# Optimization experiments

Hardware: AMD Instinct MI355X
Metric: run time of the kernel (lower is better)

The kernel has to match this reference:

```python
import jax, jax.numpy as jnp
import numpy as np
from jax import lax

Z, Y, X = 9, 5, 5          # anchor grid (AnchorInit)
A = Z * Y * X              # 225 anchors
NS = 8                     # nsample in AnchorGrouping
H = 64                     # feature / hidden width


def anchor_template():
    # (Z,Y,X,3) grid of anchor coordinates, last dim ordered (x,y,z) so that
    # anchors[:,:,:2] += g_loc shifts the planar (x,y) location.
    xs = (jnp.arange(X, dtype=jnp.float32) - (X - 1) / 2.0) * 0.2
    ys = (jnp.arange(Y, dtype=jnp.float32) - (Y - 1) / 2.0) * 0.2
    zs = jnp.arange(Z, dtype=jnp.float32) * 0.22 + 0.1
    gz, gy, gx = jnp.meshgrid(zs, ys, xs, indexing='ij')
    return jnp.stack([gx, gy, gz], axis=-1)


def setup_inputs() -> dict:
    key = jax.random.key(0)
    ks = jax.random.split(key, 16)
    B, T, N, F = 16, 64, 128, 2
    M = B * T
    s = 0.1
    f32 = jnp.float32
    return {
        'x': jax.random.normal(ks[0], (M, N, 3 + F), f32),
        'g_loc': jax.random.normal(ks[1], (B, T, 2), f32) * 0.5,
        'h0': jnp.zeros((1, B, H), f32),
        'c0': jnp.zeros((1, B, H), f32),
        # AnchorPointNet: per-point MLP 5->16->32->64 + attention pooling
        'pn_w1': jax.random.normal(ks[2], (3 + F, 16), f32) * s,
        'pn_b1': jnp.zeros((16,), f32),
        'pn_w2': jax.random.normal(ks[3], (16, 32), f32) * s,
        'pn_b2': jnp.zeros((32,), f32),
        'pn_w3': jax.random.normal(ks[4], (32, H), f32) * s,
        'pn_b3': jnp.zeros((H,), f32),
        'attn_w': jax.random.normal(ks[5], (H, 1), f32) * s,
        'attn_b': jnp.zeros((1,), f32),
        # AnchorVoxelNet: Conv3d 64->96 (3,3,3), 96->128 (3,3,3), 128->64 (5,1,1), OIDHW
        'vx_w1': jax.random.normal(ks[6], (96, 64, 3, 3, 3), f32) * s,
        'vx_b1': jnp.zeros((96,), f32),
        'vx_w2': jax.random.normal(ks[7], (128, 96, 3, 3, 3), f32) * s,
        'vx_b2': jnp.zeros((128,), f32),
        'vx_w3': jax.random.normal(ks[8], (64, 128, 5, 1, 1), f32) * s,
        'vx_b3': jnp.zeros((64,), f32),
        # AnchorRNN: 1-layer LSTM, input 64, hidden 64, torch gate order (i,f,g,o)
        'lstm_wi': jax.random.normal(ks[9], (H, 4 * H), f32) * s,
        'lstm_wh': jax.random.normal(ks[10], (H, 4 * H), f32) * s,
        'lstm_b': jnp.zeros((4 * H,), f32),
        'batch_size': 16,
        'length_size': 64,
        'feature_size': 2,
    }


def reference(x, g_loc, h0, c0,
              pn_w1, pn_b1, pn_w2, pn_b2, pn_w3, pn_b3, attn_w, attn_b,
              vx_w1, vx_b1, vx_w2, vx_b2, vx_w3, vx_b3,
              lstm_wi, lstm_wh, lstm_b,
              batch_size, length_size, feature_size):
    M = batch_size * length_size
    # ---- anchors: template grid translated by per-frame global (x,y) location
    anchors = jnp.tile(anchor_template().reshape(1, A, 3), (M, 1, 1))
    anchors = anchors.at[:, :, :2].add(g_loc.reshape(M, 1, 2))
    # ---- AnchorGrouping: 8-NN of each anchor in the radar point cloud
    xyz = x[..., :3]                      # (M,N,3)
    points = x[..., 3:]                   # (M,N,F)
    d = (jnp.sum(anchors * anchors, -1)[:, :, None]
         - 2.0 * jnp.einsum('mad,mnd->man', anchors, xyz)
         + jnp.sum(xyz * xyz, -1)[:, None, :])      # (M,A,N) squared dists
    _, idx = lax.top_k(-d, NS)                       # (M,A,8) nearest points
    bi = jnp.arange(M)[:, None, None]
    g_xyz = xyz[bi, idx] - anchors[:, :, None, :]    # (M,A,8,3) anchor-relative
    g_pts = points[bi, idx]                          # (M,A,8,F)
    grouped = jnp.concatenate([g_xyz, g_pts], -1).reshape(M * A, NS, 3 + feature_size)
    # ---- AnchorPointNet: shared MLP + attention pooling over the 8 neighbors
    f = jax.nn.relu(grouped @ pn_w1 + pn_b1)
    f = jax.nn.relu(f @ pn_w2 + pn_b2)
    f = jax.nn.relu(f @ pn_w3 + pn_b3)               # (MA,8,64)
    attn = jax.nn.softmax(f @ attn_w + attn_b, axis=1)   # (MA,8,1)
    voxel_points = jnp.sum(attn * f, axis=1)         # (MA,64)
    attn_weights = attn[..., 0]                      # (MA,8)
    # ---- AnchorVoxelNet: 3D conv over the (Z,Y,X) anchor grid
    v = voxel_points.reshape(M, Z, Y, X, H).transpose(0, 4, 1, 2, 3)  # (M,64,9,5,5)
    dn = ('NCDHW', 'OIDHW', 'NCDHW')
    v = jax.nn.relu(lax.conv_general_dilated(v, vx_w1, (1, 1, 1), 'VALID', dimension_numbers=dn)
                    + vx_b1[None, :, None, None, None])               # (M,96,7,3,3)
    v = jax.nn.relu(lax.conv_general_dilated(v, vx_w2, (1, 1, 1), 'VALID', dimension_numbers=dn)
                    + vx_b2[None, :, None, None, None])               # (M,128,5,1,1)
    v = lax.conv_general_dilated(v, vx_w3, (1, 1, 1), 'VALID', dimension_numbers=dn) \
        + vx_b3[None, :, None, None, None]                            # (M,64,1,1,1)
    voxel_vec = v.reshape(batch_size, length_size, H)
    # ---- AnchorRNN: single-layer LSTM over time
    def step(carry, xt):
        h, c = carry
        gates = xt @ lstm_wi + h @ lstm_wh + lstm_b
        i, fg, g, o = jnp.split(gates, 4, axis=-1)
        c = jax.nn.sigmoid(fg) * c + jax.nn.sigmoid(i) * jnp.tanh(g)
        h = jax.nn.sigmoid(o) * jnp.tanh(c)
        return (h, c), h
    (hn, cn), ys = lax.scan(step, (h0[0], c0[0]), voxel_vec.transpose(1, 0, 2))
    a_vec = ys.transpose(1, 0, 2)                    # (B,T,64)
    return a_vec, attn_weights, hn[None], cn[None]
```

## Files before the change

kernel.cpp:

```cpp
#include <hip/hip_runtime.h>
#include <cmath>

#define AT 225
#define NP 128
#define MT 1024
#define NSEL 8
#define HD 64

#define SZ_VOX  (1024u*64u*225u)
#define SZ_C1   (1024u*96u*63u)
#define SZ_C2   (1024u*128u*5u)
#define SZ_VV   (1024u*64u)
#define SZ_XWI  (1024u*256u)
#define SZ_W1T  (64u*27u*96u)
#define SZ_W2T  (96u*27u*128u)
#define SZ_W3T  (640u*64u)
#define SZ_W2M  (512u)

#define C2S 98

typedef __attribute__((ext_vector_type(8))) short bf16x8;
typedef __attribute__((ext_vector_type(4))) float f32x4;

__device__ __forceinline__ float sigm(float x) { return 1.0f / (1.0f + expf(-x)); }

__device__ __forceinline__ unsigned short f2bf(float f) {
    unsigned u = __float_as_uint(f);
    unsigned r = u + 0x7FFF + ((u >> 16) & 1);
    return (unsigned short)(r >> 16);
}

#if defined(__has_builtin)
#if __has_builtin(__builtin_amdgcn_cvt_pk_bf16_f32)
#define HAVE_CVT_PK_BF16 1
#endif
#endif

__device__ __forceinline__ unsigned pk2(float a, float b) {
#ifdef HAVE_CVT_PK_BF16
    auto v = __builtin_amdgcn_cvt_pk_bf16_f32(a, b);
    return __builtin_bit_cast(unsigned, v);
#else
    return (unsigned)f2bf(a) | ((unsigned)f2bf(b) << 16);
#endif
}

__global__ __launch_bounds__(256) void k_transpose(
    const float* __restrict__ w1, const float* __restrict__ w2,
    const float* __restrict__ w3, const float* __restrict__ pnw3,
    const float* __restrict__ pnw2,
    unsigned short* __restrict__ w1m, unsigned short* __restrict__ w2n,
    float* __restrict__ w3t, unsigned short* __restrict__ w3m,
    unsigned short* __restrict__ w2m)
{
    int idx = blockIdx.x * 256 + threadIdx.x;
    if (idx < 20736) {
        int lane = idx & 63, r = idx >> 6;
        int t = r % 6, s = r / 6;
        int o = t * 16 + (lane & 15);
        int kb = s * 32 + (lane >> 4) * 8;
        unsigned int dw[4];
        #pragma unroll
        for (int jd = 0; jd < 4; ++jd) {
            int k0 = kb + 2 * jd, k1 = k0 + 1;
            dw[jd] = (unsigned)f2bf(w1[o * 1728 + (k0 & 63) * 27 + (k0 >> 6)]) |
                     ((unsigned)f2bf(w1[o * 1728 + (k1 & 63) * 27 + (k1 >> 6)]) << 16);
        }
        uint4 v; v.x = dw[0]; v.y = dw[1]; v.z = dw[2]; v.w = dw[3];
        ((uint4*)w1m)[idx] = v;
    } else if (idx < 62208) {
        int q = idx - 20736;
        int lane = q & 63, r = q >> 6;
        int nt = r & 7, s = r >> 3;
        int o = nt * 16 + (lane & 15);
        int kb = s * 32 + (lane >> 4) * 8;
        unsigned int dw[4];
        #pragma unroll
        for (int jd = 0; jd < 4; ++jd) {
            int k0 = kb + 2 * jd, k1 = k0 + 1;
            dw[jd] = (unsigned)f2bf(w2[o * 2592 + (k0 % 96) * 27 + (k0 / 96)]) |
                     ((unsigned)f2bf(w2[o * 2592 + (k1 % 96) * 27 + (k1 / 96)]) << 16);
        }
        uint4 v; v.x = dw[0]; v.y = dw[1]; v.z = dw[2]; v.w = dw[3];
        ((uint4*)w2n)[q] = v;
    } else if (idx < 103168) {
        int k = idx - 62208;
        int u = k & 63, r = k >> 6;
        w3t[k] = w3[u * 640 + r];
    } else if (idx < 103424) {
        int k = idx - 103168;
        int lane = k & 63, nt = k >> 6;
        int n = nt * 16 + (lane & 15);
        int kb = (lane >> 4) * 8;
        unsigned int dw[4];
        #pragma unroll
        for (int jd = 0; jd < 4; ++jd) {
            int k0 = kb + 2 * jd;
            dw[jd] = (unsigned)f2bf(pnw3[k0 * 64 + n]) |
                     ((unsigned)f2bf(pnw3[(k0 + 1) * 64 + n]) << 16);
        }
        uint4 v; v.x = dw[0]; v.y = dw[1]; v.z = dw[2]; v.w = dw[3];
        ((uint4*)w3m)[k] = v;
    } else if (idx < 103552) {
        int k = idx - 103424;
        int lane = k & 63, nt = k >> 6;
        int n = nt * 16 + (lane & 15);
        int kb = (lane >> 4) * 8;
        unsigned int dw[4];
        #pragma unroll
        for (int jd = 0; jd < 4; ++jd) {
            int k0 = kb + 2 * jd, k1 = k0 + 1;
            float a = (k0 < 16) ? pnw2[k0 * 32 + n] : 0.0f;
            float b = (k1 < 16) ? pnw2[k1 * 32 + n] : 0.0f;
            dw[jd] = (unsigned)f2bf(a) | ((unsigned)f2bf(b) << 16);
        }
        uint4 v; v.x = dw[0]; v.y = dw[1]; v.z = dw[2]; v.w = dw[3];
        ((uint4*)w2m)[k] = v;
    }
}

__global__ __launch_bounds__(256) void k_group(
    const float* __restrict__ x, const float* __restrict__ g_loc,
    int* __restrict__ idxbuf)
{
    const int m = blockIdx.x;
    const int tid = threadIdx.x;
    __shared__ float pts[3][NP];

    for (int idx = tid; idx < NP * 5; idx += 256) {
        int n = idx / 5, c = idx % 5;
        if (c < 3) pts[c][n] = x[m * (NP * 5) + idx];
    }
    __syncthreads();

    const float gx = g_loc[m * 2 + 0], gy = g_loc[m * 2 + 1];
    const int grp = tid >> 3, li = tid & 7;

    for (int ca = 0; ca < 256; ca += 32) {
        const int a = ca + grp;
        const bool active = (a < AT);
        const int aa = active ? a : (AT - 1);
        const int azi = aa / 25, ar = aa % 25, ayi = ar / 5, axi = ar % 5;
        const float fx = ((float)axi - 2.0f) * 0.2f + gx;
        const float fy = ((float)ayi - 2.0f) * 0.2f + gy;
        const float fz = (float)azi * 0.22f + 0.1f;
        const float sa = fx * fx + fy * fy + fz * fz;

        float d[16];
        #pragma unroll
        for (int r = 0; r < 16; ++r) {
            int n = li * 16 + r;
            float px = pts[0][n], py = pts[1][n], pz = pts[2][n];
            d[r] = sa - 2.0f * (fx * px + fy * py + fz * pz)
                      + (px * px + py * py + pz * pz);
        }
        int nidx = 0;
        for (int j = 0; j < NSEL; ++j) {
            float best = 1e30f; int bidx = 0;
            #pragma unroll
            for (int r = 0; r < 16; ++r) {
                int n = li * 16 + r;
                if (d[r] < best) { best = d[r]; bidx = n; }
            }
            #pragma unroll
            for (int off = 1; off < 8; off <<= 1) {
                float ov = __shfl_xor(best, off);
                int   oi = __shfl_xor(bidx, off);
                if (ov < best || (ov == best && oi < bidx)) { best = ov; bidx = oi; }
            }
            if (li == j) nidx = bidx;
            if ((bidx >> 4) == li) {
                int slot = bidx & 15;
                #pragma unroll
                for (int r = 0; r < 16; ++r)
                    if (r == slot) d[r] = 1e30f;
            }
        }
        if (active) idxbuf[(m * AT + a) * NSEL + li] = nidx;
    }
}

__global__ __launch_bounds__(128) void k_mlpm(
    const float* __restrict__ x, const float* __restrict__ g_loc,
    const int* __restrict__ idxbuf,
    const float* __restrict__ w1, const float* __restrict__ b1,
    const unsigned short* __restrict__ w2m, const float* __restrict__ b2,
    const unsigned short* __restrict__ w3m, const float* __restrict__ b3,
    const float* __restrict__ aw, const float* __restrict__ ab,
    unsigned short* __restrict__ vox, float* __restrict__ attn_out)
{
    const int tid = threadIdx.x;
    const int row0 = blockIdx.x * 128;
    const int row = row0 + tid;

    __shared__ __align__(16) char smem[25600];
    unsigned int*   fbuf = (unsigned int*)smem;
    unsigned short* f3us = (unsigned short*)(smem + 8704);
    float*          pts  = (float*)(smem + 8704);
    float*          sbuf = (float*)smem;

    const int m0 = row0 / 1800;
    const int m1 = (row0 + 127) / 1800;
    #pragma unroll
    for (int i = tid; i < 640; i += 128) {
        pts[i]       = x[m0 * 640 + i];
        pts[640 + i] = x[m1 * 640 + i];
    }
    __syncthreads();

    const int m = row / 1800;
    const int rr = row % 1800;
    const int a = rr >> 3;
    const int base = (m == m0) ? 0 : 640;

    const int azi = a / 25, ar = a % 25, ayi = ar / 5, axi = ar % 5;
    const float gx = g_loc[m * 2 + 0], gy = g_loc[m * 2 + 1];
    const float fx = ((float)axi - 2.0f) * 0.2f + gx;
    const float fy = ((float)ayi - 2.0f) * 0.2f + gy;
    const float fz = (float)azi * 0.22f + 0.1f;

    const int nidx = idxbuf[row];
    const float in0 = pts[base + nidx * 5 + 0] - fx;
    const float in1 = pts[base + nidx * 5 + 1] - fy;
    const float in2 = pts[base + nidx * 5 + 2] - fz;
    const float in3 = pts[base + nidx * 5 + 3];
    const float in4 = pts[base + nidx * 5 + 4];

    float f1v[16];
    #pragma unroll
    for (int j = 0; j < 16; ++j) {
        float s = b1[j];
        s += in0 * w1[0 * 16 + j] + in1 * w1[1 * 16 + j] + in2 * w1[2 * 16 + j]
           + in3 * w1[3 * 16 + j] + in4 * w1[4 * 16 + j];
        f1v[j] = fmaxf(s, 0.0f);
    }
    __syncthreads();
    #pragma unroll
    for (int kd = 0; kd < 8; ++kd)
        fbuf[tid * 17 + kd] = pk2(f1v[2 * kd], f1v[2 * kd + 1]);
    #pragma unroll
    for (int kd = 8; kd < 16; ++kd)
        fbuf[tid * 17 + kd] = 0u;
    __syncthreads();

    const int wv = tid >> 6, lane = tid & 63;
    const int quad = lane >> 4, mcol = lane & 15;
    unsigned short* fus = (unsigned short*)fbuf;

    bf16x8 w2f[2];
    #pragma unroll
    for (int nt = 0; nt < 2; ++nt) {
        uint4 u = ((const uint4*)w2m)[nt * 64 + lane];
        w2f[nt] = __builtin_bit_cast(bf16x8, u);
    }
    float b2v[2] = { b2[mcol], b2[16 + mcol] };

    #pragma unroll
    for (int mt = 0; mt < 4; ++mt) {
        const int rowbase = (wv * 4 + mt) * 16;
        const int abase = (rowbase + mcol) * 17 + quad * 4;
        uint4 au;
        au.x = fbuf[abase + 0]; au.y = fbuf[abase + 1];
        au.z = fbuf[abase + 2]; au.w = fbuf[abase + 3];
        bf16x8 af = __builtin_bit_cast(bf16x8, au);
        #pragma unroll
        for (int nt = 0; nt < 2; ++nt) {
            f32x4 z = (f32x4){0.f, 0.f, 0.f, 0.f};
            f32x4 acc = __builtin_amdgcn_mfma_f32_16x16x32_bf16(af, w2f[nt], z, 0, 0, 0);
            #pragma unroll
            for (int reg = 0; reg < 4; ++reg) {
                float v = fmaxf(acc[reg] + b2v[nt], 0.0f);
                fus[(rowbase + quad * 4 + reg) * 34 + nt * 16 + mcol] = f2bf(v);
            }
        }
    }
    __syncthreads();

    bf16x8 w3f[4];
    #pragma unroll
    for (int nt = 0; nt < 4; ++nt) {
        uint4 u = ((const uint4*)w3m)[nt * 64 + lane];
        w3f[nt] = __builtin_bit_cast(bf16x8, u);
    }
    float b3v[4];
    #pragma unroll
    for (int nt = 0; nt < 4; ++nt) b3v[nt] = b3[nt * 16 + mcol];

    #pragma unroll
    for (int mt = 0; mt < 4; ++mt) {
        const int rowbase = (wv * 4 + mt) * 16;
        const int abase = (rowbase + mcol) * 17 + quad * 4;
        uint4 au;
        au.x = fbuf[abase + 0]; au.y = fbuf[abase + 1];
        au.z = fbuf[abase + 2]; au.w = fbuf[abase + 3];
        bf16x8 af = __builtin_bit_cast(bf16x8, au);
        #pragma unroll
        for (int nt = 0; nt < 4; ++nt) {
            f32x4 z = (f32x4){0.f, 0.f, 0.f, 0.f};
            f32x4 acc = __builtin_amdgcn_mfma_f32_16x16x32_bf16(af, w3f[nt], z, 0, 0, 0);
            #pragma unroll
            for (int reg = 0; reg < 4; ++reg) {
                float v = fmaxf(acc[reg] + b3v[nt], 0.0f);
                f3us[(rowbase + quad * 4 + reg) * 66 + nt * 16 + mcol] = f2bf(v);
            }
        }
    }
    __syncthreads();

    const unsigned int* f3dw = (const unsigned int*)f3us;
    float s0 = 0.f, s1 = 0.f;
    #pragma unroll
    for (int kd = 0; kd < 32; ++kd) {
        unsigned dw = f3dw[tid * 33 + kd];
        s0 = fmaf(__uint_as_float(dw << 16), aw[2 * kd], s0);
        s1 = fmaf(__uint_as_float(dw & 0xFFFF0000u), aw[2 * kd + 1], s1);
    }
    float sc = s0 + s1 + ab[0];

    float mx = sc;
    #pragma unroll
    for (int off = 1; off < 8; off <<= 1) mx = fmaxf(mx, __shfl_xor(mx, off));
    float e = expf(sc - mx);
    float den = e;
    #pragma unroll
    for (int off = 1; off < 8; off <<= 1) den += __shfl_xor(den, off);
    const float at = e / den;
    attn_out[row] = at;

    const int lgrp = tid >> 3;
    const int li = tid & 7;
    const int wl = tid & 63;
    float oo[8];
    #pragma unroll
    for (int i = 0; i < 8; ++i) oo[i] = 0.0f;
    #pragma unroll
    for (int ns = 0; ns < 8; ++ns) {
        float atn = __shfl(at, (wl >> 3) * 8 + ns);
        const int rbase = (lgrp * 8 + ns) * 33;
        #pragma unroll
        for (int q = 0; q < 4; ++q) {
            unsigned dw = f3dw[rbase + q * 8 + li];
            oo[2 * q + 0] = fmaf(atn, __uint_as_float(dw << 16), oo[2 * q + 0]);
            oo[2 * q + 1] = fmaf(atn, __uint_as_float(dw & 0xFFFF0000u), oo[2 * q + 1]);
        }
    }
    __syncthreads();
    #pragma unroll
    for (int q = 0; q < 4; ++q) {
        sbuf[lgrp * 65 + q * 16 + li * 2 + 0] = oo[2 * q + 0];
        sbuf[lgrp * 65 + q * 16 + li * 2 + 1] = oo[2 * q + 1];
    }
    __syncthreads();

    const int al = tid & 15, j = tid >> 4;
    const int ga = (row0 >> 3) + al;
    const int ma = ga / 225, aa2 = ga % 225;
    #pragma unroll
    for (int rep = 0; rep < 8; ++rep) {
        int h = j * 8 + rep;
        vox[(ma * 64 + h) * AT + aa2] = f2bf(sbuf[al * 65 + h]);
    }
}

__global__ __launch_bounds__(256) void k_conv1m(
    const unsigned short* __restrict__ vox, const unsigned short* __restrict__ w1m,
    const float* __restrict__ b1, unsigned short* __restrict__ out)
{
    const int m0 = blockIdx.x * 2;
    const int tid = threadIdx.x;
    __shared__ unsigned short voxT[2][225 * 66];

    #pragma unroll
    for (int img = 0; img < 2; ++img) {
        const unsigned int* vsrc =
            (const unsigned int*)(vox + (size_t)(m0 + img) * 14400);
        for (int i = tid; i < 7200; i += 256) {
            unsigned v = vsrc[i];
            int e0 = 2 * i, e1 = e0 + 1;
            int c0 = e0 / 225, a0 = e0 - c0 * 225;
            int c1i = e1 / 225, a1 = e1 - c1i * 225;
            voxT[img][a0 * 66 + c0] = (unsigned short)(v & 0xFFFFu);
            voxT[img][a1 * 66 + c1i] = (unsigned short)(v >> 16);
        }
    }
    __syncthreads();

    const int wv = tid >> 6, lane = tid & 63;
    const int quad = lane >> 4, n = lane & 15;
    const int p = wv * 16 + n;
    const int pe = (p > 62) ? 62 : p;
    const int zo = pe / 9, pr = pe % 9, yo = pr / 3, xo = pr % 3;
    const int basep = zo * 25 + yo * 5 + xo;

    f32x4 acc[2][6];
    #pragma unroll
    for (int g = 0; g < 2; ++g)
        #pragma unroll
        for (int t = 0; t < 6; ++t) acc[g][t] = (f32x4){0.f, 0.f, 0.f, 0.f};

    const uint4* Aptr = (const uint4*)w1m;

    auto loadB = [&](int img, int s) -> uint4 {
        int tap = s >> 1;
        int dz = tap / 9, tr = tap % 9, dy = tr / 3, dx = tr % 3;
        int rw = basep + dz * 25 + dy * 5 + dx;
        int bidx = rw * 66 + (s & 1) * 32 + quad * 8;
        const unsigned int* vp = (const unsigned int*)(&voxT[img][0] + bidx);
        uint4 r; r.x = vp[0]; r.y = vp[1]; r.z = vp[2]; r.w = vp[3];
        return r;
    };

    uint4 Acur[6], Anxt[6];
    uint4 Bcur[2], Bnxt[2];
    #pragma unroll
    for (int t = 0; t < 6; ++t) Acur[t] = Aptr[t * 64 + lane];
    Bcur[0] = loadB(0, 0); Bcur[1] = loadB(1, 0);

    for (int s = 0; s < 54; ++s) {
        if (s < 53) {
            Bnxt[0] = loadB(0, s + 1);
            Bnxt[1] = loadB(1, s + 1);
            #pragma unroll
            for (int t = 0; t < 6; ++t)
                Anxt[t] = Aptr[((s + 1) * 6 + t) * 64 + lane];
        }
        bf16x8 bf0 = __builtin_bit_cast(bf16x8, Bcur[0]);
        bf16x8 bf1 = __builtin_bit_cast(bf16x8, Bcur[1]);
        #pragma unroll
        for (int t = 0; t < 6; ++t) {
            bf16x8 af = __builtin_bit_cast(bf16x8, Acur[t]);
            acc[0][t] = __builtin_amdgcn_mfma_f32_16x16x32_bf16(af, bf0, acc[0][t], 0, 0, 0);
            acc[1][t] = __builtin_amdgcn_mfma_f32_16x16x32_bf16(af, bf1, acc[1][t], 0, 0, 0);
        }
        #pragma unroll
        for (int t = 0; t < 6; ++t) Acur[t] = Anxt[t];
        Bcur[0] = Bnxt[0]; Bcur[1] = Bnxt[1];
    }

    if (p < 63) {
        #pragma unroll
        for (int g = 0; g < 2; ++g) {
            #pragma unroll
            for (int t = 0; t < 6; ++t) {
                #pragma unroll
                for (int r = 0; r < 4; ++r) {
                    int o = t * 16 + quad * 4 + r;
                    out[(m0 + g) * (96 * 63) + o * 63 + p] =
                        f2bf(fmaxf(acc[g][t][r] + b1[o], 0.0f));
                }
            }
        }
    }
}

__global__ __launch_bounds__(256) void k_conv2m(
    const unsigned short* __restrict__ c1, const unsigned short* __restrict__ w2n,
    const float* __restrict__ b2, float* __restrict__ out)
{
    const int tid = threadIdx.x;
    const int m0 = blockIdx.x * 2;
    __shared__ unsigned short c1T[2 * 63 * C2S];

    const unsigned int* csrc = (const unsigned int*)(c1 + (size_t)m0 * 6048);
    for (int i = tid; i < 6048; i += 256) {
        unsigned v = csrc[i];
        int e0 = 2 * i;
        int mi = (i >= 3024);
        int r0 = e0 - mi * 6048, r1 = r0 + 1;
        int o0 = r0 / 63, p0 = r0 - o0 * 63;
        int o1 = r1 / 63, p1 = r1 - o1 * 63;
        c1T[(mi * 63 + p0) * C2S + o0] = (unsigned short)(v & 0xFFFFu);
        c1T[(mi * 63 + p1) * C2S + o1] = (unsigned short)(v >> 16);
    }
    __syncthreads();

    const int wv = tid >> 6, lane = tid & 63;
    const int quad = lane >> 4, ncol = lane & 15;
    const int arow = lane & 15;
    const int mi = (arow < 10) ? arow / 5 : 1;
    const int zo = (arow < 10) ? arow % 5 : 4;

    f32x4 acc[2];
    acc[0] = (f32x4){0.f, 0.f, 0.f, 0.f};
    acc[1] = (f32x4){0.f, 0.f, 0.f, 0.f};
    const uint4* Bptr = (const uint4*)w2n;

    for (int tap = 0; tap < 27; ++tap) {
        const int dz = tap / 9, r9 = tap % 9;
        const int rowb = (mi * 63 + (zo + dz) * 9 + r9) * C2S;
        #pragma unroll
        for (int sub = 0; sub < 3; ++sub) {
            const int s = tap * 3 + sub;
            const unsigned int* ap =
                (const unsigned int*)(c1T + rowb + sub * 32 + quad * 8);
            uint4 au; au.x = ap[0]; au.y = ap[1]; au.z = ap[2]; au.w = ap[3];
            bf16x8 af = __builtin_bit_cast(bf16x8, au);
            #pragma unroll
            for (int nt = 0; nt < 2; ++nt) {
                uint4 bu = Bptr[(s * 8 + wv * 2 + nt) * 64 + lane];
                bf16x8 bf = __builtin_bit_cast(bf16x8, bu);
                acc[nt] = __builtin_amdgcn_mfma_f32_16x16x32_bf16(af, bf, acc[nt], 0, 0, 0);
            }
        }
    }

    #pragma unroll
    for (int nt = 0; nt < 2; ++nt) {
        const int o = (wv * 2 + nt) * 16 + ncol;
        const float bias = b2[o];
        #pragma unroll
        for (int reg = 0; reg < 4; ++reg) {
            int rr = quad * 4 + reg;
            if (rr < 10) {
                int mg = m0 + rr / 5;
                out[mg * 640 + o * 5 + (rr % 5)] =
                    fmaxf(acc[nt][reg] + bias, 0.0f);
            }
        }
    }
}

__global__ __launch_bounds__(256) void k_c3x(
    const float* __restrict__ c2, const float* __restrict__ w3t,
    const float* __restrict__ b3, const float* __restrict__ wi,
    const float* __restrict__ lb, float* __restrict__ xwi)
{
    const int tid = threadIdx.x;
    const int m = blockIdx.x;
    __shared__ float inb[640];
    __shared__ float part[4][64];
    __shared__ float vvl[64];

    for (int i = tid; i < 640; i += 256) inb[i] = c2[m * 640 + i];
    __syncthreads();

    const int u = tid & 63, kq = tid >> 6;
    float acc = 0.0f;
    const int k0 = kq * 160;
    #pragma unroll 8
    for (int k = k0; k < k0 + 160; ++k)
        acc = fmaf(inb[k], w3t[k * 64 + u], acc);
    part[kq][u] = acc;
    __syncthreads();

    if (tid < 64)
        vvl[tid] = b3[tid] + ((part[0][tid] + part[1][tid])
                 + (part[2][tid] + part[3][tid]));
    __syncthreads();

    float a2 = lb[tid];
    #pragma unroll
    for (int k = 0; k < 64; ++k)
        a2 = fmaf(vvl[k], wi[k * 256 + tid], a2);
    xwi[m * 256 + tid] = a2;
}

__global__ __launch_bounds__(256) void k_lstm(
    const float* __restrict__ xwi, const float* __restrict__ whg,
    const float* __restrict__ h0, const float* __restrict__ c0,
    float* __restrict__ avec, float* __restrict__ hn, float* __restrict__ cn)
{
    const int b = blockIdx.x;
    const int j = threadIdx.x;
    __shared__ __align__(16) float hbuf[64];
    __shared__ float gbuf[256];

    float wh[64];
    #pragma unroll
    for (int k = 0; k < 64; ++k) wh[k] = whg[k * 256 + j];

    if (j < 64) hbuf[j] = h0[b * 64 + j];
    float c = (j < 64) ? c0[b * 64 + j] : 0.0f;
    const bool is_tanh_gate = ((j >> 6) == 2);
    __syncthreads();

    const float4* hb4 = (const float4*)hbuf;
    for (int t = 0; t < 64; ++t) {
        float g = xwi[(b * 64 + t) * 256 + j];
        float p[4] = {0.f, 0.f, 0.f, 0.f};
        #pragma unroll
        for (int k4 = 0; k4 < 16; ++k4) {
            float4 h4 = hb4[k4];
            int q = k4 & 3;
            p[q] = fmaf(h4.x, wh[4 * k4 + 0], p[q]);
            p[q] = fmaf(h4.y, wh[4 * k4 + 1], p[q]);
            p[q] = fmaf(h4.z, wh[4 * k4 + 2], p[q]);
            p[q] = fmaf(h4.w, wh[4 * k4 + 3], p[q]);
        }
        g += (p[0] + p[1]) + (p[2] + p[3]);
        gbuf[j] = is_tanh_gate ? tanhf(g) : sigm(g);
        __syncthreads();
        if (j < 64) {
            c = gbuf[64 + j] * c + gbuf[j] * gbuf[128 + j];
            float h = gbuf[192 + j] * tanhf(c);
            hbuf[j] = h;
            avec[(b * 64 + t) * 64 + j] = h;
        }
        __syncthreads();
    }
    if (j < 64) {
        hn[b * 64 + j] = hbuf[j];
        cn[b * 64 + j] = c;
    }
}

extern "C" void kernel_launch(void* const* d_in, const int* in_sizes, int n_in,
                              void* d_out, int out_size, void* d_ws, size_t ws_size,
                              hipStream_t stream) {
    const float* x     = (const float*)d_in[0];
    const float* g_loc = (const float*)d_in[1];
    const float* h0    = (const float*)d_in[2];
    const float* c0    = (const float*)d_in[3];
    const float* pn_w1 = (const float*)d_in[4];
    const float* pn_b1 = (const float*)d_in[5];
    const float* pn_w2 = (const float*)d_in[6];
    const float* pn_b2 = (const float*)d_in[7];
    const float* pn_w3 = (const float*)d_in[8];
    const float* pn_b3 = (const float*)d_in[9];
    const float* aw    = (const float*)d_in[10];
    const float* ab    = (const float*)d_in[11];
    const float* vx_w1 = (const float*)d_in[12];
    const float* vx_b1 = (const float*)d_in[13];
    const float* vx_w2 = (const float*)d_in[14];
    const float* vx_b2 = (const float*)d_in[15];
    const float* vx_w3 = (const float*)d_in[16];
    const float* vx_b3 = (const float*)d_in[17];
    const float* lwi   = (const float*)d_in[18];
    const float* lwh   = (const float*)d_in[19];
    const float* lb    = (const float*)d_in[20];

    float* ws  = (float*)d_ws;
    float* voxr = ws;
    float* c1r  = voxr + SZ_VOX;
    float* c2  = c1r + SZ_C1;
    float* vv  = c2 + SZ_C2;
    float* xwi = vv + SZ_VV;
    float* w1r = xwi + SZ_XWI;
    float* w2r = w1r + SZ_W1T;
    float* w3t = w2r + SZ_W2T;
    float* w2mr = w3t + SZ_W3T;
    unsigned short* voxh = (unsigned short*)voxr;
    unsigned short* c1h  = (unsigned short*)c1r;
    unsigned short* w1m = (unsigned short*)w1r;
    unsigned short* w2n = (unsigned short*)w2r;
    unsigned short* w2m = (unsigned short*)w2mr;
    unsigned short* w3m = (unsigned short*)xwi;
    int*   idxb = (int*)c1r;

    float* out   = (float*)d_out;
    float* avec  = out;
    float* attnw = out + 65536;
    float* hn    = out + 65536 + 1843200;
    float* cn    = hn + 1024;

    k_transpose<<<405, 256, 0, stream>>>(vx_w1, vx_w2, vx_w3, pn_w3, pn_w2,
                                         w1m, w2n, w3t, w3m, w2m);
    k_group<<<1024, 256, 0, stream>>>(x, g_loc, idxb);
    k_mlpm<<<14400, 128, 0, stream>>>(x, g_loc, idxb, pn_w1, pn_b1, w2m, pn_b2,
                                      w3m, pn_b3, aw, ab, voxh, attnw);
    k_conv1m<<<512, 256, 0, stream>>>(voxh, w1m, vx_b1, c1h);
    k_conv2m<<<512, 256, 0, stream>>>(c1h, w2n, vx_b2, c2);
    k_c3x<<<1024, 256, 0, stream>>>(c2, w3t, vx_b3, lwi, lb, xwi);
    k_lstm<<<16, 256, 0, stream>>>(xwi, lwh, h0, c0, avec, hn, cn);
}
```

Measured before the change: 358.0 us.

## Fuse conv2, conv3 and LSTM input projection into one kernel; add periodic syncs in conv1

Merges the conv2 MFMA kernel with the conv3 and input-projection kernel, so the conv2 output stays in shared memory instead of going through a global c2 buffer, and one kernel launch is removed. Each block now handles two samples for the conv3 and wi stages, reusing w3t and wi loads across both. It also inserts a __syncthreads every four steps of the conv1 MFMA loop, apparently to keep waves in lockstep for cache reuse of the shared A weights. The extra barriers may cost some latency hiding, and the fused kernel uses more shared memory.

```diff
diff --git a/kernel.cpp b/kernel.cpp
--- a/kernel.cpp
+++ b/kernel.cpp
@@ -417,6 +417,7 @@
     Bcur[0] = loadB(0, 0); Bcur[1] = loadB(1, 0);
 
     for (int s = 0; s < 54; ++s) {
+        if ((s & 3) == 0) __syncthreads();
         if (s < 53) {
             Bnxt[0] = loadB(0, s + 1);
             Bnxt[1] = loadB(1, s + 1);
@@ -453,13 +454,18 @@
     }
 }
 
-__global__ __launch_bounds__(256) void k_conv2m(
+__global__ __launch_bounds__(256) void k_c23(
     const unsigned short* __restrict__ c1, const unsigned short* __restrict__ w2n,
-    const float* __restrict__ b2, float* __restrict__ out)
+    const float* __restrict__ b2, const float* __restrict__ w3t,
+    const float* __restrict__ b3, const float* __restrict__ wi,
+    const float* __restrict__ lb, float* __restrict__ xwi)
 {
     const int tid = threadIdx.x;
     const int m0 = blockIdx.x * 2;
     __shared__ unsigned short c1T[2 * 63 * C2S];
+    __shared__ float c2l[2][640];
+    __shared__ float part[2][4][64];
+    __shared__ float vvl[2][64];
 
     const unsigned int* csrc = (const unsigned int*)(c1 + (size_t)m0 * 6048);
     for (int i = tid; i < 6048; i += 256) {
@@ -511,48 +517,40 @@
         #pragma unroll
         for (int reg = 0; reg < 4; ++reg) {
             int rr = quad * 4 + reg;
-            if (rr < 10) {
-                int mg = m0 + rr / 5;
-                out[mg * 640 + o * 5 + (rr % 5)] =
-                    fmaxf(acc[nt][reg] + bias, 0.0f);
-            }
-        }
-    }
-}
-
-__global__ __launch_bounds__(256) void k_c3x(
-    const float* __restrict__ c2, const float* __restrict__ w3t,
-    const float* __restrict__ b3, const float* __restrict__ wi,
-    const float* __restrict__ lb, float* __restrict__ xwi)
-{
-    const int tid = threadIdx.x;
-    const int m = blockIdx.x;
-    __shared__ float inb[640];
-    __shared__ float part[4][64];
-    __shared__ float vvl[64];
-
-    for (int i = tid; i < 640; i += 256) inb[i] = c2[m * 640 + i];
-    __syncthreads();
-
-    const int u = tid & 63, kq = tid >> 6;
-    float acc = 0.0f;
-    const int k0 = kq * 160;
-    #pragma unroll 8
-    for (int k = k0; k < k0 + 160; ++k)
-        acc = fmaf(inb[k], w3t[k * 64 + u], acc);
-    part[kq][u] = acc;
-    __syncthreads();
-
-    if (tid < 64)
-        vvl[tid] = b3[tid] + ((part[0][tid] + part[1][tid])
-                 + (part[2][tid] + part[3][tid]));
-    __syncthreads();
-
-    float a2 = lb[tid];
-    #pragma unroll
-    for (int k = 0; k < 64; ++k)
-        a2 = fmaf(vvl[k], wi[k * 256 + tid], a2);
-    xwi[m * 256 + tid] = a2;
+            if (rr < 10)
+                c2l[rr / 5][o * 5 + (rr % 5)] = fmaxf(acc[nt][reg] + bias, 0.0f);
+        }
+    }
+    __syncthreads();
+
+    {
+        const int u = tid & 63, kq = tid >> 6;
+        const int k0 = kq * 160;
+        #pragma unroll
+        for (int mi2 = 0; mi2 < 2; ++mi2) {
+            float acc3 = 0.0f;
+            #pragma unroll 8
+            for (int k = k0; k < k0 + 160; ++k)
+                acc3 = fmaf(c2l[mi2][k], w3t[k * 64 + u], acc3);
+            part[mi2][kq][u] = acc3;
+        }
+    }
+    __syncthreads();
+    if (tid < 128) {
+        int mi2 = tid >> 6, u = tid & 63;
+        vvl[mi2][u] = b3[u] + ((part[mi2][0][u] + part[mi2][1][u])
+                    + (part[mi2][2][u] + part[mi2][3][u]));
+    }
+    __syncthreads();
+
+    #pragma unroll
+    for (int mi2 = 0; mi2 < 2; ++mi2) {
+        float a2 = lb[tid];
+        #pragma unroll
+        for (int k = 0; k < 64; ++k)
+            a2 = fmaf(vvl[mi2][k], wi[k * 256 + tid], a2);
+        xwi[(m0 + mi2) * 256 + tid] = a2;
+    }
 }
 
 __global__ __launch_bounds__(256) void k_lstm(
@@ -659,7 +657,6 @@
     k_mlpm<<<14400, 128, 0, stream>>>(x, g_loc, idxb, pn_w1, pn_b1, w2m, pn_b2,
                                       w3m, pn_b3, aw, ab, voxh, attnw);
     k_conv1m<<<512, 256, 0, stream>>>(voxh, w1m, vx_b1, c1h);
-    k_conv2m<<<512, 256, 0, stream>>>(c1h, w2n, vx_b2, c2);
-    k_c3x<<<1024, 256, 0, stream>>>(c2, w3t, vx_b3, lwi, lb, xwi);
+    k_c23<<<512, 256, 0, stream>>>(c1h, w2n, vx_b2, w3t, vx_b3, lwi, lb, xwi);
     k_lstm<<<16, 256, 0, stream>>>(xwi, lwh, h0, c0, avec, hn, cn);
 }
```

Result: no change. 353.9 us (-1.2%).
